# Kernel optimization log

Measured on AMD Instinct MI355X. Metric: run time of the kernel, lower is better.

Reference implementation:

```python
import jax, jax.numpy as jnp
import numpy as np

N_NODES = 100000
N_FEATURES = 128
N_FILTERS = 128
N_EDGES = 3200000


def setup_inputs() -> dict:
    key = jax.random.key(0)
    k_x, k_f, k_src, k_dst, k_w = jax.random.split(key, 5)
    x = jax.random.normal(k_x, (N_NODES, N_FEATURES), dtype=jnp.float32)
    filters = jax.random.normal(k_f, (N_FEATURES, N_FILTERS), dtype=jnp.float32)
    edge_src = jax.random.randint(k_src, (N_EDGES,), 0, N_NODES, dtype=jnp.int64)
    edge_dst = jnp.sort(jax.random.randint(k_dst, (N_EDGES,), 0, N_NODES, dtype=jnp.int64))
    edge_weight = jax.random.uniform(k_w, (N_EDGES,), dtype=jnp.float32)
    return {"x": x, "filters": filters, "edge_src": edge_src,
            "edge_dst": edge_dst, "edge_weight": edge_weight}


def reference(x, filters, edge_src, edge_dst, edge_weight):
    # Dense feature transform: XF = x @ filters  -> [N, n_filters]
    XF = jnp.matmul(x, filters)
    # Sparse aggregation: out[d] += w_e * XF[s] for each edge (s, d, w_e)
    # equivalent to torch.sparse.mm(transform, XF) with transform in COO form.
    msgs = XF[edge_src] * edge_weight[:, None]           # [E, n_filters]
    out = jax.ops.segment_sum(msgs, edge_dst, num_segments=N_NODES)
    return out
```

## Files before the change

kernel.cpp:

```cpp
#include <hip/hip_runtime.h>
#include <stdint.h>

#define N_NODES 100000
#define N_FEAT 128
#define N_EDGES 3200000

static __device__ __forceinline__ unsigned int f2bf_u(float f) {
    unsigned int u = __float_as_uint(f);
    u += 0x7FFFu + ((u >> 16) & 1u);
    return u >> 16;
}

typedef __bf16 bf16x8 __attribute__((ext_vector_type(8)));
typedef float f32x4 __attribute__((ext_vector_type(4)));

__global__ __launch_bounds__(256) void k_prep(
        const float* __restrict__ x, unsigned int* __restrict__ xi8,
        float* __restrict__ xscale,
        const float* __restrict__ f, unsigned short* __restrict__ fT,
        const int* __restrict__ dst, int* __restrict__ row_ptr) {
    int b = blockIdx.x;
    if (b < 12500) {
        int wave = threadIdx.x >> 6, lane = threadIdx.x & 63;
        int l32 = lane & 31;
        int node = b * 8 + wave * 2 + (lane >> 5);
        float4 v = *(const float4*)(x + (size_t)node * 128 + l32 * 4);
        float am = fmaxf(fmaxf(fabsf(v.x), fabsf(v.y)), fmaxf(fabsf(v.z), fabsf(v.w)));
        for (int d = 1; d < 32; d <<= 1) am = fmaxf(am, __shfl_xor(am, d));
        float s = am * (1.f / 127.f);
        float inv = 127.f / fmaxf(am, 1e-20f);
        int q0 = (int)rintf(v.x * inv), q1 = (int)rintf(v.y * inv);
        int q2 = (int)rintf(v.z * inv), q3 = (int)rintf(v.w * inv);
        xi8[(size_t)node * 32 + l32] = (unsigned int)((q0 & 0xFF) | ((q1 & 0xFF) << 8) |
                                                      ((q2 & 0xFF) << 16) | ((q3 & 0xFF) << 24));
        if (l32 == 0) xscale[node] = s;
    } else if (b < 25000) {
        int e = (b - 12500) * 256 + threadIdx.x;
        if (e >= N_EDGES) return;
        int dcur = dst[e];
        if (e == 0) {
            for (int d = 0; d <= dcur; ++d) row_ptr[d] = 0;
        } else {
            int dprev = dst[e - 1];
            for (int d = dprev + 1; d <= dcur; ++d) row_ptr[d] = e;
        }
        if (e == N_EDGES - 1) {
            for (int d = dcur + 1; d <= N_NODES; ++d) row_ptr[d] = N_EDGES;
        }
    } else {
        int i = (b - 25000) * 256 + threadIdx.x;
        if (i >= N_FEAT * N_FEAT) return;
        int k = i >> 7, n = i & 127;
        fT[n * N_FEAT + k] = (unsigned short)f2bf_u(f[i]);
    }
}

#define LDA 136
#define LDC 132

__global__ __launch_bounds__(512, 4) void k_agg_gemm(
        const unsigned int* __restrict__ xi8,
        const float* __restrict__ xscale,
        const int* __restrict__ src,
        const float* __restrict__ w,
        const int* __restrict__ row_ptr,
        const unsigned short* __restrict__ BT,
        float* __restrict__ C) {
    __shared__ uint4 lds[3520];
    uint2*          smeta = (uint2*)lds;
    unsigned short* Abuf  = (unsigned short*)((char*)lds + 4096);
    unsigned short* Bbuf  = (unsigned short*)((char*)lds + 4096 + 17408);
    float*          Cbuf  = (float*)lds;

    int t = threadIdx.x;
    int wave = t >> 6, lane = t & 63;
    int base = blockIdx.x * 64;

    for (int i = 0; i < 4; ++i) {
        int idx = t + i * 512;
        int r = idx >> 4, c8 = idx & 15;
        *(uint4*)(Bbuf + r * LDA + c8 * 8) = *(const uint4*)(BT + r * 128 + c8 * 8);
    }

    int half = lane >> 5, ffeat = lane & 31;
    for (int n = 0; n < 8; ++n) {
        int node = base + wave * 8 + n;
        if (node >= N_NODES) break;
        int start = row_ptr[node], end = row_ptr[node + 1];
        float a0 = 0.f, a1 = 0.f, a2 = 0.f, a3 = 0.f;
        for (int e0 = start; e0 < end; e0 += 64) {
            int e = e0 + lane;
            uint2 m = make_uint2(0u, 0u);
            if (e < end) {
                int sv = src[e];
                m.x = (unsigned int)sv;
                m.y = __float_as_uint(w[e] * xscale[sv]);
            }
            smeta[wave * 64 + lane] = m;
            int cnt16 = (min(64, end - e0) + 15) & ~15;
            for (int j = 0; j < cnt16; j += 16) {
                unsigned int vv[8]; float wj[8];
#pragma unroll
                for (int u = 0; u < 8; ++u) {
                    uint2 mm = smeta[wave * 64 + j + u * 2 + half];
                    wj[u] = __uint_as_float(mm.y);
                    vv[u] = xi8[mm.x * 32 + ffeat];
                }
#pragma unroll
                for (int u = 0; u < 8; ++u) {
                    int s32 = (int)vv[u];
                    a0 = fmaf(wj[u], (float)((s32 << 24) >> 24), a0);
                    a1 = fmaf(wj[u], (float)((s32 << 16) >> 24), a1);
                    a2 = fmaf(wj[u], (float)((s32 <<  8) >> 24), a2);
                    a3 = fmaf(wj[u], (float)( s32        >> 24), a3);
                }
            }
        }
        a0 += __shfl_xor(a0, 32);
        a1 += __shfl_xor(a1, 32);
        a2 += __shfl_xor(a2, 32);
        a3 += __shfl_xor(a3, 32);
        if (half == 0) {
            uint2 o;
            o.x = (f2bf_u(a1) << 16) | f2bf_u(a0);
            o.y = (f2bf_u(a3) << 16) | f2bf_u(a2);
            *(uint2*)(Abuf + (wave * 8 + n) * LDA + ffeat * 4) = o;
        }
    }
    __syncthreads();

    int m15 = lane & 15, q = lane >> 4;
    f32x4 acc[4];
    for (int i = 0; i < 4; ++i) acc[i] = f32x4{0.f, 0.f, 0.f, 0.f};
    for (int kk = 0; kk < 128; kk += 32) {
        bf16x8 bfr = *(const bf16x8*)(Bbuf + (wave * 16 + m15) * LDA + kk + q * 8);
#pragma unroll
        for (int i = 0; i < 4; ++i) {
            bf16x8 afr = *(const bf16x8*)(Abuf + (i * 16 + m15) * LDA + kk + q * 8);
            acc[i] = __builtin_amdgcn_mfma_f32_16x16x32_bf16(afr, bfr, acc[i], 0, 0, 0);
        }
    }
    __syncthreads();

    for (int i = 0; i < 4; ++i)
#pragma unroll
        for (int r = 0; r < 4; ++r)
            Cbuf[(i * 16 + q * 4 + r) * LDC + wave * 16 + m15] = acc[i][r];
    __syncthreads();
    for (int it = 0; it < 4; ++it) {
        int idx = t + it * 512;
        int row = idx >> 5, c4 = (idx & 31) * 4;
        int grow = base + row;
        if (grow < N_NODES)
            *(float4*)(C + (size_t)grow * 128 + c4) = *(const float4*)(Cbuf + row * LDC + c4);
    }
}

extern "C" void kernel_launch(void* const* d_in, const int* in_sizes, int n_in,
                              void* d_out, int out_size, void* d_ws, size_t ws_size,
                              hipStream_t stream) {
    const float* x        = (const float*)d_in[0];
    const float* filters  = (const float*)d_in[1];
    const int*   edge_src = (const int*)d_in[2];
    const int*   edge_dst = (const int*)d_in[3];
    const float* edge_w   = (const float*)d_in[4];
    float* out = (float*)d_out;

    char* ws = (char*)d_ws;
    unsigned int*   xi8  = (unsigned int*)  (ws);
    float*          xsc  = (float*)         (ws + 13ll * 1024 * 1024);
    unsigned short* fT   = (unsigned short*)(ws + 14ll * 1024 * 1024);
    int*            rp   = (int*)           (ws + 15ll * 1024 * 1024);

    hipLaunchKernelGGL(k_prep, dim3(25064), dim3(256), 0, stream,
                       x, xi8, xsc, filters, fT, edge_dst, rp);
    hipLaunchKernelGGL(k_agg_gemm, dim3(1563), dim3(512), 0, stream,
                       xi8, xsc, edge_src, edge_w, rp, fT, out);
}
```

Before: 232.2 us.

## Split fused aggregate-GEMM kernel into separate aggregation and MFMA GEMM kernels

Splits the fused aggregate-then-GEMM kernel into two kernels. The aggregation kernel uses one wave per node with small blocks and writes bf16 aggregated rows to a workspace buffer. A separate GEMM kernel loads a pre-swizzled bf16 filter layout (produced in prep) into LDS and runs MFMA per 64-row tile. The aim is better occupancy and load balance for the gather phase than the 512-thread fused block with a large LDS footprint. In exchange it adds a kernel launch and a global round trip of the intermediate bf16 activations (about 25 MB written and read).

After: 200.9 us. -13.5%, faster.

```diff
diff --git a/kernel.cpp b/kernel.cpp
--- a/kernel.cpp
+++ b/kernel.cpp
@@ -17,7 +17,7 @@
 __global__ __launch_bounds__(256) void k_prep(
         const float* __restrict__ x, unsigned int* __restrict__ xi8,
         float* __restrict__ xscale,
-        const float* __restrict__ f, unsigned short* __restrict__ fT,
+        const float* __restrict__ f, unsigned short* __restrict__ fB,
         const int* __restrict__ dst, int* __restrict__ row_ptr) {
     int b = blockIdx.x;
     if (b < 12500) {
@@ -50,110 +50,103 @@
     } else {
         int i = (b - 25000) * 256 + threadIdx.x;
         if (i >= N_FEAT * N_FEAT) return;
-        int k = i >> 7, n = i & 127;
-        fT[n * N_FEAT + k] = (unsigned short)f2bf_u(f[i]);
+        int n = ((i >> 11) << 4) | ((i >> 3) & 15);
+        int k = (((i >> 9) & 3) << 5) | (((i >> 7) & 3) << 3) | (i & 7);
+        fB[i] = (unsigned short)f2bf_u(f[k * 128 + n]);
     }
 }
 
-#define LDA 136
-#define LDC 132
-
-__global__ __launch_bounds__(512, 4) void k_agg_gemm(
+__global__ __launch_bounds__(256) void k_aggregate(
         const unsigned int* __restrict__ xi8,
         const float* __restrict__ xscale,
         const int* __restrict__ src,
         const float* __restrict__ w,
         const int* __restrict__ row_ptr,
-        const unsigned short* __restrict__ BT,
+        unsigned int* __restrict__ aggb) {
+    __shared__ uint2 smeta[4][64];
+    int wave = threadIdx.x >> 6, lane = threadIdx.x & 63;
+    int node = blockIdx.x * 4 + wave;
+    if (node >= N_NODES) return;
+    int half = lane >> 5, f = lane & 31;
+    int start = row_ptr[node], end = row_ptr[node + 1];
+    float a0 = 0.f, a1 = 0.f, a2 = 0.f, a3 = 0.f;
+
+    for (int e0 = start; e0 < end; e0 += 64) {
+        int e = e0 + lane;
+        uint2 m = make_uint2(0u, 0u);
+        if (e < end) {
+            int sv = src[e];
+            m.x = (unsigned int)sv;
+            m.y = __float_as_uint(w[e] * xscale[sv]);
+        }
+        smeta[wave][lane] = m;
+        int cnt16 = (min(64, end - e0) + 15) & ~15;
+        for (int j = 0; j < cnt16; j += 16) {
+            unsigned int vv[8]; float wj[8];
+#pragma unroll
+            for (int u = 0; u < 8; ++u) {
+                uint2 mm = smeta[wave][j + u * 2 + half];
+                wj[u] = __uint_as_float(mm.y);
+                vv[u] = xi8[mm.x * 32 + f];
+            }
+#pragma unroll
+            for (int u = 0; u < 8; ++u) {
+                int s32 = (int)vv[u];
+                a0 = fmaf(wj[u], (float)((s32 << 24) >> 24), a0);
+                a1 = fmaf(wj[u], (float)((s32 << 16) >> 24), a1);
+                a2 = fmaf(wj[u], (float)((s32 <<  8) >> 24), a2);
+                a3 = fmaf(wj[u], (float)( s32        >> 24), a3);
+            }
+        }
+    }
+    a0 += __shfl_xor(a0, 32);
+    a1 += __shfl_xor(a1, 32);
+    a2 += __shfl_xor(a2, 32);
+    a3 += __shfl_xor(a3, 32);
+    if (half == 0) {
+        uint2 o;
+        o.x = (f2bf_u(a1) << 16) | f2bf_u(a0);
+        o.y = (f2bf_u(a3) << 16) | f2bf_u(a2);
+        *(uint2*)(aggb + (size_t)node * 64 + f * 2) = o;
+    }
+}
+
+__global__ __launch_bounds__(256) void k_gemm(
+        const unsigned short* __restrict__ A,
+        const unsigned short* __restrict__ fB,
         float* __restrict__ C) {
-    __shared__ uint4 lds[3520];
-    uint2*          smeta = (uint2*)lds;
-    unsigned short* Abuf  = (unsigned short*)((char*)lds + 4096);
-    unsigned short* Bbuf  = (unsigned short*)((char*)lds + 4096 + 17408);
-    float*          Cbuf  = (float*)lds;
+    __shared__ unsigned short Bbuf[16384];
+    int t = threadIdx.x;
+    for (int i = 0; i < 8; ++i)
+        ((uint4*)Bbuf)[t + i * 256] = ((const uint4*)fB)[t + i * 256];
+    __syncthreads();
 
-    int t = threadIdx.x;
-    int wave = t >> 6, lane = t & 63;
-    int base = blockIdx.x * 64;
+    int wave = t >> 6, lane = t & 63, m15 = lane & 15, q = lane >> 4;
+    int row = blockIdx.x * 64 + wave * 16 + m15;
+    int rowc = min(row, N_NODES - 1);
 
-    for (int i = 0; i < 4; ++i) {
-        int idx = t + i * 512;
-        int r = idx >> 4, c8 = idx & 15;
-        *(uint4*)(Bbuf + r * LDA + c8 * 8) = *(const uint4*)(BT + r * 128 + c8 * 8);
+    f32x4 acc[8];
+#pragma unroll
+    for (int j = 0; j < 8; ++j) acc[j] = f32x4{0.f, 0.f, 0.f, 0.f};
+
+#pragma unroll
+    for (int kkidx = 0; kkidx < 4; ++kkidx) {
+        bf16x8 a = *(const bf16x8*)(A + (size_t)rowc * 128 + kkidx * 32 + q * 8);
+#pragma unroll
+        for (int j = 0; j < 8; ++j) {
+            bf16x8 b = *(const bf16x8*)(Bbuf + (((j * 4 + kkidx) * 64 + lane) * 8));
+            acc[j] = __builtin_amdgcn_mfma_f32_16x16x32_bf16(a, b, acc[j], 0, 0, 0);
+        }
     }
 
-    int half = lane >> 5, ffeat = lane & 31;
-    for (int n = 0; n < 8; ++n) {
-        int node = base + wave * 8 + n;
-        if (node >= N_NODES) break;
-        int start = row_ptr[node], end = row_ptr[node + 1];
-        float a0 = 0.f, a1 = 0.f, a2 = 0.f, a3 = 0.f;
-        for (int e0 = start; e0 < end; e0 += 64) {
-            int e = e0 + lane;
-            uint2 m = make_uint2(0u, 0u);
-            if (e < end) {
-                int sv = src[e];
-                m.x = (unsigned int)sv;
-                m.y = __float_as_uint(w[e] * xscale[sv]);
-            }
-            smeta[wave * 64 + lane] = m;
-            int cnt16 = (min(64, end - e0) + 15) & ~15;
-            for (int j = 0; j < cnt16; j += 16) {
-                unsigned int vv[8]; float wj[8];
+    int rowbase = blockIdx.x * 64 + wave * 16 + q * 4;
 #pragma unroll
-                for (int u = 0; u < 8; ++u) {
-                    uint2 mm = smeta[wave * 64 + j + u * 2 + half];
-                    wj[u] = __uint_as_float(mm.y);
-                    vv[u] = xi8[mm.x * 32 + ffeat];
-                }
-#pragma unroll
-                for (int u = 0; u < 8; ++u) {
-                    int s32 = (int)vv[u];
-                    a0 = fmaf(wj[u], (float)((s32 << 24) >> 24), a0);
-                    a1 = fmaf(wj[u], (float)((s32 << 16) >> 24), a1);
-                    a2 = fmaf(wj[u], (float)((s32 <<  8) >> 24), a2);
-                    a3 = fmaf(wj[u], (float)( s32        >> 24), a3);
-                }
-            }
+    for (int j = 0; j < 8; ++j)
+        for (int r = 0; r < 4; ++r) {
+            int gr = rowbase + r;
+            if (gr < N_NODES)
+                C[(size_t)gr * 128 + j * 16 + m15] = acc[j][r];
         }
-        a0 += __shfl_xor(a0, 32);
-        a1 += __shfl_xor(a1, 32);
-        a2 += __shfl_xor(a2, 32);
-        a3 += __shfl_xor(a3, 32);
-        if (half == 0) {
-            uint2 o;
-            o.x = (f2bf_u(a1) << 16) | f2bf_u(a0);
-            o.y = (f2bf_u(a3) << 16) | f2bf_u(a2);
-            *(uint2*)(Abuf + (wave * 8 + n) * LDA + ffeat * 4) = o;
-        }
-    }
-    __syncthreads();
-
-    int m15 = lane & 15, q = lane >> 4;
-    f32x4 acc[4];
-    for (int i = 0; i < 4; ++i) acc[i] = f32x4{0.f, 0.f, 0.f, 0.f};
-    for (int kk = 0; kk < 128; kk += 32) {
-        bf16x8 bfr = *(const bf16x8*)(Bbuf + (wave * 16 + m15) * LDA + kk + q * 8);
-#pragma unroll
-        for (int i = 0; i < 4; ++i) {
-            bf16x8 afr = *(const bf16x8*)(Abuf + (i * 16 + m15) * LDA + kk + q * 8);
-            acc[i] = __builtin_amdgcn_mfma_f32_16x16x32_bf16(afr, bfr, acc[i], 0, 0, 0);
-        }
-    }
-    __syncthreads();
-
-    for (int i = 0; i < 4; ++i)
-#pragma unroll
-        for (int r = 0; r < 4; ++r)
-            Cbuf[(i * 16 + q * 4 + r) * LDC + wave * 16 + m15] = acc[i][r];
-    __syncthreads();
-    for (int it = 0; it < 4; ++it) {
-        int idx = t + it * 512;
-        int row = idx >> 5, c4 = (idx & 31) * 4;
-        int grow = base + row;
-        if (grow < N_NODES)
-            *(float4*)(C + (size_t)grow * 128 + c4) = *(const float4*)(Cbuf + row * LDC + c4);
-    }
 }
 
 extern "C" void kernel_launch(void* const* d_in, const int* in_sizes, int n_in,
@@ -169,11 +162,14 @@
     char* ws = (char*)d_ws;
     unsigned int*   xi8  = (unsigned int*)  (ws);
     float*          xsc  = (float*)         (ws + 13ll * 1024 * 1024);
-    unsigned short* fT   = (unsigned short*)(ws + 14ll * 1024 * 1024);
-    int*            rp   = (int*)           (ws + 15ll * 1024 * 1024);
+    unsigned int*   aggb = (unsigned int*)  (ws + 14ll * 1024 * 1024);
+    unsigned short* fB   = (unsigned short*)(ws + 40ll * 1024 * 1024);
+    int*            rp   = (int*)           (ws + 41ll * 1024 * 1024);
 
     hipLaunchKernelGGL(k_prep, dim3(25064), dim3(256), 0, stream,
-                       x, xi8, xsc, filters, fT, edge_dst, rp);
-    hipLaunchKernelGGL(k_agg_gemm, dim3(1563), dim3(512), 0, stream,
-                       xi8, xsc, edge_src, edge_w, rp, fT, out);
+                       x, xi8, xsc, filters, fB, edge_dst, rp);
+    hipLaunchKernelGGL(k_aggregate, dim3(25000), dim3(256), 0, stream,
+                       xi8, xsc, edge_src, edge_w, rp, aggb);
+    hipLaunchKernelGGL(k_gemm, dim3(1563), dim3(256), 0, stream,
+                       (const unsigned short*)aggb, fB, out);
 }
```
